# Kernel optimization log

Measured on AMD Instinct MI355X. Metric: run time of the kernel, lower is better.

Reference implementation:

```python
import jax, jax.numpy as jnp
import numpy as np

N_NODES = 50000
N_EDGES = 800000
IN_DIM = 6
HID = 256
OUT = 256
N_EXPERTS = 8
N_LAYERS = 2
N_GRAPHS = 64


def setup_inputs() -> dict:
    key = jax.random.key(0)
    ks = jax.random.split(key, 16)
    s = 0.05
    x = jax.random.normal(ks[0], (N_NODES, IN_DIM), dtype=jnp.float32)
    edge_index = jax.random.randint(ks[1], (2, N_EDGES), 0, N_NODES, dtype=jnp.int64)
    batch = jnp.sort(jax.random.randint(ks[2], (N_NODES,), 0, N_GRAPHS, dtype=jnp.int64))
    # shared encoder
    W_enc = jax.random.normal(ks[3], (IN_DIM, HID), jnp.float32) * s
    b_enc = jnp.zeros((HID,), jnp.float32)
    # router MLP: (HID+2) -> HID -> N_EXPERTS
    Wr1 = jax.random.normal(ks[4], (HID + 2, HID), jnp.float32) * s
    br1 = jnp.zeros((HID,), jnp.float32)
    Wr2 = jax.random.normal(ks[5], (HID, N_EXPERTS), jnp.float32) * s
    br2 = jnp.zeros((N_EXPERTS,), jnp.float32)
    # experts: 2 GraphConv layers each (self weight + neighbor weight + bias), stacked over experts
    Ws0 = jax.random.normal(ks[6], (N_EXPERTS, HID, HID), jnp.float32) * s
    Wn0 = jax.random.normal(ks[7], (N_EXPERTS, HID, HID), jnp.float32) * s
    b0 = jnp.zeros((N_EXPERTS, HID), jnp.float32)
    Ws1 = jax.random.normal(ks[8], (N_EXPERTS, HID, OUT), jnp.float32) * s
    Wn1 = jax.random.normal(ks[9], (N_EXPERTS, HID, OUT), jnp.float32) * s
    b1 = jnp.zeros((N_EXPERTS, OUT), jnp.float32)
    return dict(x=x, edge_index=edge_index, batch=batch, W_enc=W_enc, b_enc=b_enc,
                Wr1=Wr1, br1=br1, Wr2=Wr2, br2=br2,
                Ws0=Ws0, Wn0=Wn0, b0=b0, Ws1=Ws1, Wn1=Wn1, b1=b1)


def _graph_conv(h, src, dst, Ws, Wn, b):
    # PyG GraphConv: x' = x @ Ws + sum_{j in N(i)} x_j @ Wn + b
    msg = h[src] @ Wn                                   # [E, d_out]
    agg = jax.ops.segment_sum(msg, dst, num_segments=N_NODES)
    return h @ Ws + agg + b


def reference(x, edge_index, batch, W_enc, b_enc, Wr1, br1, Wr2, br2,
              Ws0, Wn0, b0, Ws1, Wn1, b1):
    src, dst = edge_index[0], edge_index[1]
    # shared encoder
    h = jax.nn.relu(x @ W_enc + b_enc)                  # [N, HID]
    # graph size features: per-graph node count and edge count, log-scaled, broadcast to nodes
    ones_n = jnp.ones((h.shape[0],), h.dtype)
    node_cnt = jax.ops.segment_sum(ones_n, batch, num_segments=N_GRAPHS)
    edge_cnt = jax.ops.segment_sum(jnp.ones((src.shape[0],), h.dtype), batch[src], num_segments=N_GRAPHS)
    size_feat = jnp.stack([jnp.log1p(node_cnt)[batch], jnp.log1p(edge_cnt)[batch]], axis=-1)  # [N, 2]
    # router -> top-1 expert index
    r = jax.nn.relu(jnp.concatenate([h, size_feat], axis=-1) @ Wr1 + br1)
    logits = r @ Wr2 + br2                              # [N, n_experts]
    idx = jnp.argmax(logits, axis=-1)                   # [N]
    # dense compute-all-experts, then gather by argmax (faithful to original)
    out = jnp.zeros((h.shape[0], Ws1.shape[-1]), h.dtype)
    for e in range(N_EXPERTS):
        z = jax.nn.relu(_graph_conv(h, src, dst, Ws0[e], Wn0[e], b0[e]))
        y_e = _graph_conv(z, src, dst, Ws1[e], Wn1[e], b1[e])   # [N, OUT]
        out = out + jnp.where((idx == e)[:, None], y_e, 0.0)
    return out
```

## Files before the change

### kernel.cpp

```cpp
#include <hip/hip_runtime.h>
#include <hip/hip_bf16.h>
#include <math.h>

#define NN 50000
#define NE 800000
#define NG 64
#define NEXP 8

typedef __attribute__((ext_vector_type(8))) short bf16x8;
typedef __attribute__((ext_vector_type(4))) float f32x4;
typedef unsigned short ushort_t;

__device__ __forceinline__ unsigned short f2bf(float f) {
  union { float f; unsigned u; } x; x.f = f;
  unsigned r = x.u + 0x7fff + ((x.u >> 16) & 1);
  return (unsigned short)(r >> 16);
}
__device__ __forceinline__ float bf2f(unsigned short u) {
  union { unsigned u; float f; } x; x.u = ((unsigned)u) << 16; return x.f;
}

__device__ __forceinline__ void gld16(const void* g, void* l) {
  __builtin_amdgcn_global_load_lds(
      (const __attribute__((address_space(1))) unsigned int*)g,
      (__attribute__((address_space(3))) unsigned int*)l, 16, 0, 0);
}

__global__ __launch_bounds__(256) void k_encoder(
    const float* __restrict__ x, const float* __restrict__ W,
    const float* __restrict__ b, ushort_t* __restrict__ Xb,
    ushort_t* __restrict__ Xlo) {
  int i = blockIdx.x, n = threadIdx.x;
  float acc = b[n];
#pragma unroll
  for (int k = 0; k < 6; k++) acc = fmaf(x[i * 6 + k], W[k * 256 + n], acc);
  acc = fmaxf(acc, 0.f);
  unsigned short hb = f2bf(acc);
  Xb[(size_t)i * 512 + n] = hb;
  Xlo[(size_t)i * 256 + n] = f2bf(acc - bf2f(hb));
}

__global__ __launch_bounds__(256) void k_count_nodes(
    const int* __restrict__ batch, int* __restrict__ node_cnt) {
  __shared__ int bins[NG];
  int t = threadIdx.x;
  if (t < NG) bins[t] = 0;
  __syncthreads();
  for (int i = blockIdx.x * blockDim.x + t; i < NN; i += gridDim.x * blockDim.x)
    atomicAdd(&bins[batch[i]], 1);
  __syncthreads();
  if (t < NG) atomicAdd(&node_cnt[t], bins[t]);
}

__global__ __launch_bounds__(256) void k_count_edges(
    const int* __restrict__ ei, const int* __restrict__ batch,
    int* __restrict__ edge_cnt, int* __restrict__ deg) {
  __shared__ int bins[NG];
  int t = threadIdx.x;
  if (t < NG) bins[t] = 0;
  __syncthreads();
  for (int e = blockIdx.x * blockDim.x + t; e < NE; e += gridDim.x * blockDim.x) {
    int s = ei[e];
    int d = ei[NE + e];
    atomicAdd(&bins[batch[s]], 1);
    atomicAdd(&deg[d], 1);
  }
  __syncthreads();
  if (t < NG) atomicAdd(&edge_cnt[t], bins[t]);
}

__global__ __launch_bounds__(256) void k_sizefeat(
    const int* __restrict__ batch, const int* __restrict__ node_cnt,
    const int* __restrict__ edge_cnt, float* __restrict__ sf0,
    float* __restrict__ sf1) {
  int i = blockIdx.x * blockDim.x + threadIdx.x;
  if (i < NN) {
    int g = batch[i];
    sf0[i] = log1pf((float)node_cnt[g]);
    sf1[i] = log1pf((float)edge_cnt[g]);
  }
}

__global__ __launch_bounds__(1024) void k_scan(
    const int* __restrict__ deg, int* __restrict__ offs, int* __restrict__ cursor) {
  __shared__ int wsums[16];
  int t = threadIdx.x, lane = t & 63, wid = t >> 6;
  int carry = 0;
  for (int base = 0; base < NN; base += 1024) {
    int i = base + t;
    int v = (i < NN) ? deg[i] : 0;
    int x = v;
#pragma unroll
    for (int d = 1; d < 64; d <<= 1) {
      int y = __shfl_up(x, d, 64);
      if (lane >= d) x += y;
    }
    if (lane == 63) wsums[wid] = x;
    __syncthreads();
    if (wid == 0) {
      int s = (lane < 16) ? wsums[lane] : 0;
#pragma unroll
      for (int d = 1; d < 16; d <<= 1) {
        int y = __shfl_up(s, d, 64);
        if (lane >= d) s += y;
      }
      if (lane < 16) wsums[lane] = s;
    }
    __syncthreads();
    int wpre = (wid > 0) ? wsums[wid - 1] : 0;
    int excl = carry + wpre + x - v;
    if (i < NN) { offs[i] = excl; cursor[i] = excl; }
    int btot = wsums[15];
    __syncthreads();
    carry += btot;
  }
  if (t == 0) offs[NN] = carry;
}

__global__ __launch_bounds__(256) void k_fill_csr(
    const int* __restrict__ ei, int* __restrict__ cursor, int* __restrict__ edge_src) {
  int e = blockIdx.x * blockDim.x + threadIdx.x;
  if (e < NE) {
    int d = ei[NE + e];
    int pos = atomicAdd(&cursor[d], 1);
    edge_src[pos] = ei[e];
  }
}

__global__ __launch_bounds__(256) void k_agg_h2(
    const int* __restrict__ offs, const int* __restrict__ edge_src,
    ushort_t* __restrict__ Xb) {
  int wid = threadIdx.x >> 6, lane = threadIdx.x & 63;
  int half = lane >> 5, cl = lane & 31;
  int i = blockIdx.x * 4 + wid;
  if (i >= NN) return;
  int e0 = offs[i], e1 = offs[i + 1];
  float acc[8] = {};
  int k = e0;
  for (; k + 8 <= e1; k += 8) {
    int s0 = edge_src[k + half];
    int s1 = edge_src[k + 2 + half];
    int s2 = edge_src[k + 4 + half];
    int s3 = edge_src[k + 6 + half];
    bf16x8 v0 = *(const bf16x8*)&Xb[(size_t)s0 * 512 + cl * 8];
    bf16x8 v1 = *(const bf16x8*)&Xb[(size_t)s1 * 512 + cl * 8];
    bf16x8 v2 = *(const bf16x8*)&Xb[(size_t)s2 * 512 + cl * 8];
    bf16x8 v3 = *(const bf16x8*)&Xb[(size_t)s3 * 512 + cl * 8];
#pragma unroll
    for (int j = 0; j < 8; j++) acc[j] += bf2f((unsigned short)v0[j]);
#pragma unroll
    for (int j = 0; j < 8; j++) acc[j] += bf2f((unsigned short)v1[j]);
#pragma unroll
    for (int j = 0; j < 8; j++) acc[j] += bf2f((unsigned short)v2[j]);
#pragma unroll
    for (int j = 0; j < 8; j++) acc[j] += bf2f((unsigned short)v3[j]);
  }
  for (; k + 2 <= e1; k += 2) {
    int s0 = edge_src[k + half];
    bf16x8 v0 = *(const bf16x8*)&Xb[(size_t)s0 * 512 + cl * 8];
#pragma unroll
    for (int j = 0; j < 8; j++) acc[j] += bf2f((unsigned short)v0[j]);
  }
  if (k < e1 && half == 0) {
    int s0 = edge_src[k];
    bf16x8 v0 = *(const bf16x8*)&Xb[(size_t)s0 * 512 + cl * 8];
#pragma unroll
    for (int j = 0; j < 8; j++) acc[j] += bf2f((unsigned short)v0[j]);
  }
#pragma unroll
  for (int j = 0; j < 8; j++) acc[j] += __shfl_xor(acc[j], 32, 64);
  if (half == 0) {
    bf16x8 o;
#pragma unroll
    for (int j = 0; j < 8; j++) o[j] = (short)f2bf(acc[j]);
    *(bf16x8*)(&Xb[(size_t)i * 512 + 256 + cl * 8]) = o;
  }
}

__global__ __launch_bounds__(256) void k_prep_w(
    const float* __restrict__ Ws0, const float* __restrict__ Wn0,
    const float* __restrict__ Ws1, const float* __restrict__ Wn1,
    ushort_t* __restrict__ Wt1, ushort_t* __restrict__ Wt2) {
  __shared__ float tile[32][33];
  int z = blockIdx.z;
  int e = z & 7;
  const float* Ws = (z < 8) ? Ws0 : Ws1;
  const float* Wn = (z < 8) ? Wn0 : Wn1;
  ushort_t* Wt = (z < 8) ? Wt1 : Wt2;
  int kt = blockIdx.x;
  int nt = blockIdx.y;
  int tx = threadIdx.x & 31, ty = threadIdx.x >> 5;
  const float* src = (kt < 8) ? (Ws + e * 65536 + (kt * 32) * 256)
                              : (Wn + e * 65536 + ((kt - 8) * 32) * 256);
#pragma unroll
  for (int rr = 0; rr < 32; rr += 8) {
    int k = rr + ty;
    tile[k][tx] = src[k * 256 + nt * 32 + tx];
  }
  __syncthreads();
#pragma unroll
  for (int rr = 0; rr < 32; rr += 8) {
    int n = rr + ty;
    Wt[(size_t)e * 131072 + (nt * 32 + n) * 512 + kt * 32 + tx] = f2bf(tile[tx][n]);
  }
}

__global__ __launch_bounds__(256) void k_prep_wr1(
    const float* __restrict__ Wr1, ushort_t* __restrict__ Wr1t) {
  int k = blockIdx.x;
  int n = threadIdx.x;
  unsigned short v;
  if (k < 256) {
    v = f2bf(Wr1[k * 256 + n]);
  } else {
    float f = Wr1[(k - 256) * 256 + n];
    unsigned short h = f2bf(f);
    v = f2bf(f - bf2f(h));
  }
  Wr1t[(size_t)n * 512 + k] = v;
}

#define TIE_TAU 1e-4f
__global__ __launch_bounds__(256) void k_router_mfma(
    const ushort_t* __restrict__ Xb,
    const ushort_t* __restrict__ Xlo,
    const ushort_t* __restrict__ Wr1t,
    const float* __restrict__ Wr1, const float* __restrict__ br1,
    const float* __restrict__ Wr2, const float* __restrict__ sf0,
    const float* __restrict__ sf1, float* __restrict__ Lpart) {
  __shared__ ushort_t As[2][4096];
  __shared__ ushort_t Bs1[2][4096];
  __shared__ ushort_t Bs2[2][4096];
  __shared__ float Lsm[128][NEXP];
  int t = threadIdx.x;
  int w = t >> 6, lane = t & 63;
  int m0 = blockIdx.x * 128;
  int n0 = blockIdx.y * 128;
  int wm = w >> 1, wn = w & 1;
  int q16 = lane >> 4, c15 = lane & 15;
  for (int z = t; z < 128 * NEXP; z += 256) ((float*)Lsm)[z] = 0.f;

  auto STAGE = [&](int s, int kt) {
    int k0 = (kt & 7) * 32;
    bool hi = kt < 8;
#pragma unroll
    for (int i = 0; i < 2; i++) {
      int c = w * 128 + i * 64 + lane;
      int ch = c >> 7, r = c & 127;
      int gr = m0 + r; if (gr >= NN) gr = NN - 1;
      int dst = (w * 128 + i * 64) * 8;
      if (hi) {
        gld16(Xb + (size_t)gr * 512 + k0 + ch * 8, (void*)&As[s][dst]);
        gld16(Wr1t + (size_t)(n0 + r) * 512 + k0 + ch * 8, (void*)&Bs1[s][dst]);
        gld16(Wr1t + (size_t)(n0 + r) * 512 + 256 + k0 + ch * 8, (void*)&Bs2[s][dst]);
      } else {
        gld16(Xlo + (size_t)gr * 256 + k0 + ch * 8, (void*)&As[s][dst]);
        gld16(Wr1t + (size_t)(n0 + r) * 512 + k0 + ch * 8, (void*)&Bs1[s][dst]);
      }
    }
  };

  f32x4 acc[4][4] = {};
  STAGE(0, 0);
  __syncthreads();
  for (int kt = 0; kt < 16; kt++) {
    int cur = kt & 1;
    if (kt < 15) STAGE(cur ^ 1, kt + 1);
    bf16x8 a[4], b1[4];
#pragma unroll
    for (int i = 0; i < 4; i++) {
      int ra = wm * 64 + i * 16 + c15;
      a[i] = *(const bf16x8*)&As[cur][q16 * 1024 + ra * 8];
      int nb = wn * 64 + i * 16 + c15;
      b1[i] = *(const bf16x8*)&Bs1[cur][q16 * 1024 + nb * 8];
    }
#pragma unroll
    for (int i = 0; i < 4; i++)
#pragma unroll
      for (int j = 0; j < 4; j++)
        acc[i][j] = __builtin_amdgcn_mfma_f32_16x16x32_bf16(a[i], b1[j], acc[i][j], 0, 0, 0);
    if (kt < 8) {
      bf16x8 b2[4];
#pragma unroll
      for (int i = 0; i < 4; i++) {
        int nb = wn * 64 + i * 16 + c15;
        b2[i] = *(const bf16x8*)&Bs2[cur][q16 * 1024 + nb * 8];
      }
#pragma unroll
      for (int i = 0; i < 4; i++)
#pragma unroll
        for (int j = 0; j < 4; j++)
          acc[i][j] = __builtin_amdgcn_mfma_f32_16x16x32_bf16(a[i], b2[j], acc[i][j], 0, 0, 0);
    }
    __syncthreads();
  }

  float bb[4], w6[4], w7[4];
#pragma unroll
  for (int j = 0; j < 4; j++) {
    int col = n0 + wn * 64 + j * 16 + c15;
    bb[j] = br1[col];
    w6[j] = Wr1[65536 + col];
    w7[j] = Wr1[65792 + col];
  }
#pragma unroll
  for (int i = 0; i < 4; i++)
#pragma unroll
    for (int v = 0; v < 4; v++) {
      int row = m0 + wm * 64 + i * 16 + q16 * 4 + v;
      float s0v = (row < NN) ? sf0[row] : 0.f;
      float s1v = (row < NN) ? sf1[row] : 0.f;
#pragma unroll
      for (int j = 0; j < 4; j++)
        acc[i][j][v] = fmaxf(acc[i][j][v] + bb[j] + s0v * w6[j] + s1v * w7[j], 0.f);
    }
#pragma unroll
  for (int e = 0; e < NEXP; e++) {
    float wr2j[4];
#pragma unroll
    for (int j = 0; j < 4; j++)
      wr2j[j] = Wr2[(n0 + wn * 64 + j * 16 + c15) * 8 + e];
    float pe[4][4];
#pragma unroll
    for (int i = 0; i < 4; i++)
#pragma unroll
      for (int v = 0; v < 4; v++) {
        float s = acc[i][0][v] * wr2j[0];
        s = fmaf(acc[i][1][v], wr2j[1], s);
        s = fmaf(acc[i][2][v], wr2j[2], s);
        s = fmaf(acc[i][3][v], wr2j[3], s);
        pe[i][v] = s;
      }
#pragma unroll
    for (int d = 1; d < 16; d <<= 1)
#pragma unroll
      for (int i = 0; i < 4; i++)
#pragma unroll
        for (int v = 0; v < 4; v++)
          pe[i][v] += __shfl_xor(pe[i][v], d, 64);
    if (c15 == 0) {
#pragma unroll
      for (int i = 0; i < 4; i++)
#pragma unroll
        for (int v = 0; v < 4; v++)
          atomicAdd(&Lsm[wm * 64 + i * 16 + q16 * 4 + v][e], pe[i][v]);
    }
  }
  __syncthreads();
  for (int z = t; z < 128 * NEXP; z += 256) {
    int lr = z >> 3, e = z & 7;
    int row = m0 + lr;
    if (row < NN)
      Lpart[(size_t)blockIdx.y * (NN * 8) + (size_t)row * 8 + e] = Lsm[lr][e];
  }
}

__global__ __launch_bounds__(256) void k_argmax(
    const float* __restrict__ Lpart, const float* __restrict__ br2,
    int* __restrict__ idx, int* __restrict__ nfix, int* __restrict__ fixlist) {
  int i = blockIdx.x * 256 + threadIdx.x;
  if (i >= NN) return;
  float best = -1e30f, second = -1e30f; int bi = 0;
#pragma unroll
  for (int e = 0; e < NEXP; e++) {
    float v = br2[e] + Lpart[(size_t)i * 8 + e]
              + Lpart[(size_t)(NN * 8) + (size_t)i * 8 + e];
    if (v > best) { second = best; best = v; bi = e; }
    else if (v > second) second = v;
  }
  idx[i] = bi;
  if (best - second < TIE_TAU) {
    int p = atomicAdd(nfix, 1);
    fixlist[p] = i;
  }
}

__global__ __launch_bounds__(256) void k_fixup(
    const float* __restrict__ x, const float* __restrict__ W_enc,
    const float* __restrict__ b_enc, const float* __restrict__ Wr1,
    const float* __restrict__ br1, const float* __restrict__ Wr2,
    const float* __restrict__ br2, const float* __restrict__ sf0,
    const float* __restrict__ sf1, const int* __restrict__ fixlist,
    const int* __restrict__ nfix, int* __restrict__ idx) {
  __shared__ float hsh[256];
  __shared__ float lred[4][NEXP];
  int n = *nfix;
  int t = threadIdx.x, wid = t >> 6, lane = t & 63;
  for (int qq = blockIdx.x; qq < n; qq += gridDim.x) {
    int node = fixlist[qq];
    float hv = b_enc[t];
#pragma unroll
    for (int k = 0; k < 6; k++)
      hv = fmaf(x[node * 6 + k], W_enc[k * 256 + t], hv);
    hsh[t] = fmaxf(hv, 0.f);
    __syncthreads();
    float acc = br1[t] + sf0[node] * Wr1[65536 + t] + sf1[node] * Wr1[65792 + t];
    for (int k = 0; k < 256; k++)
      acc = fmaf(hsh[k], Wr1[k * 256 + t], acc);
    float r = fmaxf(acc, 0.f);
    float le[NEXP];
#pragma unroll
    for (int e = 0; e < NEXP; e++) le[e] = r * Wr2[t * 8 + e];
#pragma unroll
    for (int d = 32; d > 0; d >>= 1)
#pragma unroll
      for (int e = 0; e < NEXP; e++) le[e] += __shfl_xor(le[e], d, 64);
    if (lane == 0) {
#pragma unroll
      for (int e = 0; e < NEXP; e++) lred[wid][e] = le[e];
    }
    __syncthreads();
    if (t == 0) {
      float best = -1e30f; int bi = 0;
      for (int e = 0; e < NEXP; e++) {
        float v = lred[0][e] + lred[1][e] + lred[2][e] + lred[3][e] + br2[e];
        if (v > best) { best = v; bi = e; }
      }
      idx[node] = bi;
    }
    __syncthreads();
  }
}

__global__ __launch_bounds__(256) void k_ecnt(
    const int* __restrict__ idx, int* __restrict__ ecnt) {
  __shared__ int bins[NEXP];
  int t = threadIdx.x;
  if (t < NEXP) bins[t] = 0;
  __syncthreads();
  for (int i = blockIdx.x * 256 + t; i < NN; i += gridDim.x * 256)
    atomicAdd(&bins[idx[i]], 1);
  __syncthreads();
  if (t < NEXP) atomicAdd(&ecnt[t], bins[t]);
}

__global__ __launch_bounds__(256) void k_srcmask(
    const int* __restrict__ ei, const int* __restrict__ idx,
    unsigned int* __restrict__ mask) {
  int k = blockIdx.x * 256 + threadIdx.x;
  if (k < NE) {
    int s = ei[k], d = ei[NE + k];
    atomicOr(&mask[s], 1u << idx[d]);
  }
  if (k < NN) atomicOr(&mask[k], 1u << idx[k]);
}

__global__ __launch_bounds__(256) void k_scount(
    const unsigned int* __restrict__ mask, int* __restrict__ scnt) {
  __shared__ int bins[NEXP];
  int t = threadIdx.x;
  if (t < NEXP) bins[t] = 0;
  __syncthreads();
  for (int i = blockIdx.x * 256 + t; i < NN; i += gridDim.x * 256) {
    unsigned m = mask[i];
    while (m) { int b = __ffs(m) - 1; atomicAdd(&bins[b], 1); m &= m - 1; }
  }
  __syncthreads();
  if (t < NEXP) atomicAdd(&scnt[t], bins[t]);
}

__global__ void k_bucket_offs(const int* __restrict__ ecnt,
                              const int* __restrict__ scnt,
                              int* __restrict__ boff, int* __restrict__ bcur,
                              int* __restrict__ tstart,
                              int* __restrict__ soff, int* __restrict__ scur) {
  if (threadIdx.x == 0) {
    int s = 0, ts = 0, s2 = 0;
    for (int e = 0; e < NEXP; e++) {
      boff[e] = s; bcur[e] = s;
      tstart[e] = ts;
      ts += (ecnt[e] + 127) / 128;
      s += ecnt[e];
      soff[e] = s2; scur[e] = s2;
      s2 += scnt[e];
    }
    boff[NEXP] = s;
    tstart[NEXP] = ts;
    soff[NEXP] = s2;
  }
}

#define BF_BLOCKS 64
__global__ __launch_bounds__(256) void k_bucket_fill2(
    const int* __restrict__ idx, int* __restrict__ bcur, int* __restrict__ nlist) {
  __shared__ int lcnt[NEXP];
  __shared__ int lbase[NEXP];
  int t = threadIdx.x;
  int chunk = (NN + BF_BLOCKS - 1) / BF_BLOCKS;
  int lo = blockIdx.x * chunk;
  int hi = lo + chunk; if (hi > NN) hi = NN;
  if (t < NEXP) lcnt[t] = 0;
  __syncthreads();
  for (int i = lo + t; i < hi; i += 256) atomicAdd(&lcnt[idx[i]], 1);
  __syncthreads();
  if (t < NEXP) lbase[t] = atomicAdd(&bcur[t], lcnt[t]);
  __syncthreads();
  if (t < NEXP) lcnt[t] = 0;
  __syncthreads();
  for (int i = lo + t; i < hi; i += 256) {
    int e = idx[i];
    int p = atomicAdd(&lcnt[e], 1);
    nlist[lbase[e] + p] = i;
  }
}

__global__ __launch_bounds__(256) void k_scompact(
    const unsigned int* __restrict__ mask, int* __restrict__ scur,
    int* __restrict__ slist) {
  __shared__ int lcnt[NEXP];
  __shared__ int lbase[NEXP];
  int t = threadIdx.x;
  int chunk = (NN + BF_BLOCKS - 1) / BF_BLOCKS;
  int lo = blockIdx.x * chunk;
  int hi = lo + chunk; if (hi > NN) hi = NN;
  if (t < NEXP) lcnt[t] = 0;
  __syncthreads();
  for (int i = lo + t; i < hi; i += 256) {
    unsigned m = mask[i];
    while (m) { int b = __ffs(m) - 1; atomicAdd(&lcnt[b], 1); m &= m - 1; }
  }
  __syncthreads();
  if (t < NEXP) lbase[t] = atomicAdd(&scur[t], lcnt[t]);
  __syncthreads();
  if (t < NEXP) lcnt[t] = 0;
  __syncthreads();
  for (int i = lo + t; i < hi; i += 256) {
    unsigned m = mask[i];
    while (m) {
      int b = __ffs(m) - 1;
      int p = atomicAdd(&lcnt[b], 1);
      slist[lbase[b] + p] = i;
      m &= m - 1;
    }
  }
}

__global__ __launch_bounds__(256) void k_layer1_rows(
    const ushort_t* __restrict__ Abf,
    const ushort_t* __restrict__ Wt,
    const float* __restrict__ b0, const int* __restrict__ idx,
    const int* __restrict__ slist, const int* __restrict__ soff, int e,
    ushort_t* __restrict__ Zb, ushort_t* __restrict__ A2) {
  int base = soff[e];
  int cnt = soff[e + 1] - base;
  int m0 = blockIdx.x * 128;
  if (m0 >= cnt) return;
  __shared__ ushort_t As[2][4096];
  __shared__ ushort_t Bs[2][4096];
  __shared__ int rows[128];
  __shared__ int sidx[128];
  int t = threadIdx.x;
  if (t < 128) {
    int r = (m0 + t < cnt) ? slist[base + m0 + t] : -1;
    rows[t] = r;
    sidx[t] = (r >= 0) ? idx[r] : -1;
  }
  __syncthreads();
  int w = t >> 6, lane = t & 63;
  int n0 = blockIdx.y * 128;
  int wm = w >> 1, wn = w & 1;
  int q16 = lane >> 4, c15 = lane & 15;
  const ushort_t* Wb = Wt + (size_t)e * 131072;

  auto STAGE = [&](int s, int kt) {
    int k0 = kt * 32;
#pragma unroll
    for (int i = 0; i < 2; i++) {
      int c = w * 128 + i * 64 + lane;
      int ch = c >> 7, r = c & 127;
      int nd = rows[r]; if (nd < 0) nd = 0;
      int dst = (w * 128 + i * 64) * 8;
      gld16(Abf + (size_t)nd * 512 + k0 + ch * 8, (void*)&As[s][dst]);
      gld16(Wb + (size_t)(n0 + r) * 512 + k0 + ch * 8, (void*)&Bs[s][dst]);
    }
  };

  f32x4 acc[4][4] = {};
  STAGE(0, 0);
  __syncthreads();
  for (int kt = 0; kt < 16; kt++) {
    int cur = kt & 1;
    if (kt < 15) STAGE(cur ^ 1, kt + 1);
    bf16x8 a[4], b[4];
#pragma unroll
    for (int i = 0; i < 4; i++) {
      int ra = wm * 64 + i * 16 + c15;
      a[i] = *(const bf16x8*)&As[cur][q16 * 1024 + ra * 8];
      int nb = wn * 64 + i * 16 + c15;
      b[i] = *(const bf16x8*)&Bs[cur][q16 * 1024 + nb * 8];
    }
#pragma unroll
    for (int i = 0; i < 4; i++)
#pragma unroll
      for (int j = 0; j < 4; j++)
        acc[i][j] = __builtin_amdgcn_mfma_f32_16x16x32_bf16(a[i], b[j], acc[i][j], 0, 0, 0);
    __syncthreads();
  }
  int q = lane >> 4;
#pragma unroll
  for (int i = 0; i < 4; i++) {
#pragma unroll
    for (int j = 0; j < 4; j++) {
      int col = n0 + wn * 64 + j * 16 + c15;
      float bias = b0[e * 256 + col];
#pragma unroll
      for (int v = 0; v < 4; v++) {
        int lrow = wm * 64 + i * 16 + q * 4 + v;
        int node = rows[lrow];
        if (node >= 0) {
          unsigned short zb = f2bf(fmaxf(acc[i][j][v] + bias, 0.f));
          Zb[(size_t)node * 256 + col] = zb;
          if (sidx[lrow] == e) A2[(size_t)node * 512 + col] = zb;
        }
      }
    }
  }
}

__global__ __launch_bounds__(256) void k_agg_z2(
    const ushort_t* __restrict__ Zb, const int* __restrict__ offs,
    const int* __restrict__ edge_src, const int* __restrict__ nlist,
    const int* __restrict__ boff, int e, ushort_t* __restrict__ A2) {
  int wid = threadIdx.x >> 6, lane = threadIdx.x & 63;
  int half = lane >> 5, cl = lane & 31;
  int base = boff[e];
  int cnt = boff[e + 1] - base;
  for (int b = blockIdx.x * 4 + wid; b < cnt; b += gridDim.x * 4) {
    int i = nlist[base + b];
    int e0 = offs[i], e1 = offs[i + 1];
    float acc[8] = {};
    int k = e0;
    for (; k + 8 <= e1; k += 8) {
      int s0 = edge_src[k + half];
      int s1 = edge_src[k + 2 + half];
      int s2 = edge_src[k + 4 + half];
      int s3 = edge_src[k + 6 + half];
      bf16x8 v0 = *(const bf16x8*)&Zb[(size_t)s0 * 256 + cl * 8];
      bf16x8 v1 = *(const bf16x8*)&Zb[(size_t)s1 * 256 + cl * 8];
      bf16x8 v2 = *(const bf16x8*)&Zb[(size_t)s2 * 256 + cl * 8];
      bf16x8 v3 = *(const bf16x8*)&Zb[(size_t)s3 * 256 + cl * 8];
#pragma unroll
      for (int j = 0; j < 8; j++) acc[j] += bf2f((unsigned short)v0[j]);
#pragma unroll
      for (int j = 0; j < 8; j++) acc[j] += bf2f((unsigned short)v1[j]);
#pragma unroll
      for (int j = 0; j < 8; j++) acc[j] += bf2f((unsigned short)v2[j]);
#pragma unroll
      for (int j = 0; j < 8; j++) acc[j] += bf2f((unsigned short)v3[j]);
    }
    for (; k + 2 <= e1; k += 2) {
      int s0 = edge_src[k + half];
      bf16x8 v0 = *(const bf16x8*)&Zb[(size_t)s0 * 256 + cl * 8];
#pragma unroll
      for (int j = 0; j < 8; j++) acc[j] += bf2f((unsigned short)v0[j]);
    }
    if (k < e1 && half == 0) {
      int s0 = edge_src[k];
      bf16x8 v0 = *(const bf16x8*)&Zb[(size_t)s0 * 256 + cl * 8];
#pragma unroll
      for (int j = 0; j < 8; j++) acc[j] += bf2f((unsigned short)v0[j]);
    }
#pragma unroll
    for (int j = 0; j < 8; j++) acc[j] += __shfl_xor(acc[j], 32, 64);
    if (half == 0) {
      bf16x8 o;
#pragma unroll
      for (int j = 0; j < 8; j++) o[j] = (short)f2bf(acc[j]);
      *(bf16x8*)(&A2[(size_t)i * 512 + 256 + cl * 8]) = o;
    }
  }
}

#define MAXT2 (391 + NEXP)
__global__ __launch_bounds__(256) void k_layer2_mfma(
    const ushort_t* __restrict__ A2,
    const ushort_t* __restrict__ Wt,
    const float* __restrict__ b1, const int* __restrict__ nlist,
    const int* __restrict__ boff, const int* __restrict__ tstart,
    float* __restrict__ outp) {
  __shared__ ushort_t As[2][4096];
  __shared__ ushort_t Bs[2][4096];
  __shared__ int rows[128];
  int t = threadIdx.x;
  int tx = blockIdx.x;
  int e = -1;
#pragma unroll
  for (int q = 0; q < NEXP; q++)
    if (tx >= tstart[q] && tx < tstart[q + 1]) e = q;
  if (e < 0) return;
  int tile = tx - tstart[e];
  int base = boff[e];
  int cnt = boff[e + 1] - base;
  int m0 = tile * 128;
  if (t < 128) rows[t] = (m0 + t < cnt) ? nlist[base + m0 + t] : -1;
  __syncthreads();
  int w = t >> 6, lane = t & 63;
  int n0 = blockIdx.y * 128;
  int wm = w >> 1, wn = w & 1;
  int q16 = lane >> 4, c15 = lane & 15;
  const ushort_t* Wb = Wt + (size_t)e * 131072;

  auto STAGE = [&](int s, int kt) {
    int k0 = kt * 32;
#pragma unroll
    for (int i = 0; i < 2; i++) {
      int c = w * 128 + i * 64 + lane;
      int ch = c >> 7, r = c & 127;
      int nd = rows[r]; if (nd < 0) nd = 0;
      int dst = (w * 128 + i * 64) * 8;
      gld16(A2 + (size_t)nd * 512 + k0 + ch * 8, (void*)&As[s][dst]);
      gld16(Wb + (size_t)(n0 + r) * 512 + k0 + ch * 8, (void*)&Bs[s][dst]);
    }
  };

  f32x4 acc[4][4] = {};
  STAGE(0, 0);
  __syncthreads();
  for (int kt = 0; kt < 16; kt++) {
    int cur = kt & 1;
    if (kt < 15) STAGE(cur ^ 1, kt + 1);
    bf16x8 a[4], b[4];
#pragma unroll
    for (int i = 0; i < 4; i++) {
      int ra = wm * 64 + i * 16 + c15;
      a[i] = *(const bf16x8*)&As[cur][q16 * 1024 + ra * 8];
      int nb = wn * 64 + i * 16 + c15;
      b[i] = *(const bf16x8*)&Bs[cur][q16 * 1024 + nb * 8];
    }
#pragma unroll
    for (int i = 0; i < 4; i++)
#pragma unroll
      for (int j = 0; j < 4; j++)
        acc[i][j] = __builtin_amdgcn_mfma_f32_16x16x32_bf16(a[i], b[j], acc[i][j], 0, 0, 0);
    __syncthreads();
  }
  int q = lane >> 4;
#pragma unroll
  for (int i = 0; i < 4; i++) {
#pragma unroll
    for (int j = 0; j < 4; j++) {
      int col = n0 + wn * 64 + j * 16 + c15;
      float bias = b1[e * 256 + col];
#pragma unroll
      for (int v = 0; v < 4; v++) {
        int lrow = wm * 64 + i * 16 + q * 4 + v;
        int node = rows[lrow];
        if (node >= 0) outp[(size_t)node * 256 + col] = acc[i][j][v] + bias;
      }
    }
  }
}

static inline char* wsalloc(char*& p, size_t bytes) {
  char* r = p;
  p += (bytes + 255) & ~(size_t)255;
  return r;
}

extern "C" void kernel_launch(void* const* d_in, const int* in_sizes, int n_in,
                              void* d_out, int out_size, void* d_ws, size_t ws_size,
                              hipStream_t stream) {
  const float* x     = (const float*)d_in[0];
  const int*   ei    = (const int*)d_in[1];
  const int*   batch = (const int*)d_in[2];
  const float* W_enc = (const float*)d_in[3];
  const float* b_enc = (const float*)d_in[4];
  const float* Wr1   = (const float*)d_in[5];
  const float* br1   = (const float*)d_in[6];
  const float* Wr2   = (const float*)d_in[7];
  const float* br2   = (const float*)d_in[8];
  const float* Ws0   = (const float*)d_in[9];
  const float* Wn0   = (const float*)d_in[10];
  const float* b0    = (const float*)d_in[11];
  const float* Ws1   = (const float*)d_in[12];
  const float* Wn1   = (const float*)d_in[13];
  const float* b1    = (const float*)d_in[14];
  float* outp = (float*)d_out;

  char* p = (char*)d_ws;
  ushort_t* Xb   = (ushort_t*)wsalloc(p, (size_t)NN * 512 * 2);
  ushort_t* Zb   = (ushort_t*)wsalloc(p, (size_t)NN * 256 * 2);
  ushort_t* A2   = (ushort_t*)wsalloc(p, (size_t)NN * 512 * 2);
  ushort_t* Xlo  = Zb;
  float*    Lpart= (float*)wsalloc(p, (size_t)2 * NN * 8 * 4);
  ushort_t* Wt1  = (ushort_t*)wsalloc(p, (size_t)NEXP * 256 * 512 * 2);
  ushort_t* Wt2  = (ushort_t*)wsalloc(p, (size_t)NEXP * 256 * 512 * 2);
  ushort_t* Wr1t = (ushort_t*)wsalloc(p, (size_t)256 * 512 * 2);
  int* edge_src  = (int*)wsalloc(p, (size_t)NE * 4);
  int* offs      = (int*)wsalloc(p, (size_t)(NN + 1) * 4);
  int* cursor    = (int*)wsalloc(p, (size_t)NN * 4);
  int* deg       = (int*)wsalloc(p, (size_t)NN * 4);
  int* idxb      = (int*)wsalloc(p, (size_t)NN * 4);
  float* sf0     = (float*)wsalloc(p, (size_t)NN * 4);
  float* sf1     = (float*)wsalloc(p, (size_t)NN * 4);
  int* nlist     = (int*)wsalloc(p, (size_t)NN * 4);
  int* fixlist   = (int*)wsalloc(p, (size_t)NN * 4);
  unsigned int* maskb = (unsigned int*)wsalloc(p, (size_t)NN * 4);
  int* slist     = (int*)wsalloc(p, (size_t)NN * NEXP * 4);
  int* smallb    = (int*)wsalloc(p, 256 * 4);
  int* node_cnt = smallb;
  int* edge_cnt = smallb + 64;
  int* ecnt     = smallb + 128;
  int* boff     = smallb + 136;
  int* bcur     = smallb + 152;
  int* tstart   = smallb + 160;
  int* nfix     = smallb + 192;
  int* scnt     = smallb + 200;
  int* soff     = smallb + 208;
  int* scur     = smallb + 224;

  hipMemsetAsync(deg, 0, (size_t)NN * 4, stream);
  hipMemsetAsync(smallb, 0, 256 * 4, stream);
  hipMemsetAsync(maskb, 0, (size_t)NN * 4, stream);

  k_encoder<<<NN, 256, 0, stream>>>(x, W_enc, b_enc, Xb, Xlo);
  k_count_nodes<<<64, 256, 0, stream>>>(batch, node_cnt);
  k_count_edges<<<128, 256, 0, stream>>>(ei, batch, edge_cnt, deg);
  k_sizefeat<<<(NN + 255) / 256, 256, 0, stream>>>(batch, node_cnt, edge_cnt, sf0, sf1);
  k_scan<<<1, 1024, 0, stream>>>(deg, offs, cursor);
  k_fill_csr<<<(NE + 255) / 256, 256, 0, stream>>>(ei, cursor, edge_src);
  k_agg_h2<<<(NN + 3) / 4, 256, 0, stream>>>(offs, edge_src, Xb);
  k_prep_w<<<dim3(16, 8, 16), 256, 0, stream>>>(Ws0, Wn0, Ws1, Wn1, Wt1, Wt2);
  k_prep_wr1<<<512, 256, 0, stream>>>(Wr1, Wr1t);
  k_router_mfma<<<dim3((NN + 127) / 128, 2), 256, 0, stream>>>(
      Xb, Xlo, Wr1t, Wr1, br1, Wr2, sf0, sf1, Lpart);
  k_argmax<<<(NN + 255) / 256, 256, 0, stream>>>(Lpart, br2, idxb, nfix, fixlist);
  k_fixup<<<256, 256, 0, stream>>>(x, W_enc, b_enc, Wr1, br1, Wr2, br2,
                                   sf0, sf1, fixlist, nfix, idxb);
  k_srcmask<<<(NE + 255) / 256, 256, 0, stream>>>(ei, idxb, maskb);
  k_ecnt<<<64, 256, 0, stream>>>(idxb, ecnt);
  k_scount<<<64, 256, 0, stream>>>(maskb, scnt);
  k_bucket_offs<<<1, 64, 0, stream>>>(ecnt, scnt, boff, bcur, tstart, soff, scur);
  k_bucket_fill2<<<BF_BLOCKS, 256, 0, stream>>>(idxb, bcur, nlist);
  k_scompact<<<BF_BLOCKS, 256, 0, stream>>>(maskb, scur, slist);
  for (int e = 0; e < NEXP; e++) {
    k_layer1_rows<<<dim3((NN + 127) / 128, 2), 256, 0, stream>>>(
        Xb, Wt1, b0, idxb, slist, soff, e, Zb, A2);
    k_agg_z2<<<3125, 256, 0, stream>>>(Zb, offs, edge_src, nlist, boff, e, A2);
  }
  k_layer2_mfma<<<dim3(MAXT2, 2), 256, 0, stream>>>(
      A2, Wt2, b1, nlist, boff, tstart, outp);
}
```

Before: 691.3 us.

## Fuse per-expert layer1/aggregation loop into single launches with compacted Z buffer and LDS swizzle

The eight-iteration expert loop of layer-1 GEMM plus neighbor aggregation becomes one layer-1 kernel covering all experts' tiles and one aggregation kernel over all nodes. Layer-1 outputs go to a compacted Zc buffer indexed through a per-expert position map. The launches are fewer, the GPU fills better, and the separate per-expert passes disappear. Separately, all MFMA GEMM LDS tiles switch to a row-major XOR-swizzled layout to cut bank conflicts. The compacted buffer is capped at 3*NN rows and overflow positions fall back to index 0, which silently gives wrong results if the source-mask sets exceed the cap.

```diff
diff --git a/kernel.cpp b/kernel.cpp
--- a/kernel.cpp
+++ b/kernel.cpp
@@ -6,6 +6,7 @@
 #define NE 800000
 #define NG 64
 #define NEXP 8
+#define ZC_CAP (3 * NN)
 
 typedef __attribute__((ext_vector_type(8))) short bf16x8;
 typedef __attribute__((ext_vector_type(4))) float f32x4;
@@ -246,16 +247,17 @@
 #pragma unroll
     for (int i = 0; i < 2; i++) {
       int c = w * 128 + i * 64 + lane;
-      int ch = c >> 7, r = c & 127;
+      int r = c >> 2, kc = c & 3;
+      int kcs = kc ^ (r & 3);
       int gr = m0 + r; if (gr >= NN) gr = NN - 1;
       int dst = (w * 128 + i * 64) * 8;
       if (hi) {
-        gld16(Xb + (size_t)gr * 512 + k0 + ch * 8, (void*)&As[s][dst]);
-        gld16(Wr1t + (size_t)(n0 + r) * 512 + k0 + ch * 8, (void*)&Bs1[s][dst]);
-        gld16(Wr1t + (size_t)(n0 + r) * 512 + 256 + k0 + ch * 8, (void*)&Bs2[s][dst]);
+        gld16(Xb + (size_t)gr * 512 + k0 + kcs * 8, (void*)&As[s][dst]);
+        gld16(Wr1t + (size_t)(n0 + r) * 512 + k0 + kcs * 8, (void*)&Bs1[s][dst]);
+        gld16(Wr1t + (size_t)(n0 + r) * 512 + 256 + k0 + kcs * 8, (void*)&Bs2[s][dst]);
       } else {
-        gld16(Xlo + (size_t)gr * 256 + k0 + ch * 8, (void*)&As[s][dst]);
-        gld16(Wr1t + (size_t)(n0 + r) * 512 + k0 + ch * 8, (void*)&Bs1[s][dst]);
+        gld16(Xlo + (size_t)gr * 256 + k0 + kcs * 8, (void*)&As[s][dst]);
+        gld16(Wr1t + (size_t)(n0 + r) * 512 + k0 + kcs * 8, (void*)&Bs1[s][dst]);
       }
     }
   };
@@ -270,9 +272,9 @@
 #pragma unroll
     for (int i = 0; i < 4; i++) {
       int ra = wm * 64 + i * 16 + c15;
-      a[i] = *(const bf16x8*)&As[cur][q16 * 1024 + ra * 8];
+      a[i] = *(const bf16x8*)&As[cur][ra * 32 + (q16 ^ (ra & 3)) * 8];
       int nb = wn * 64 + i * 16 + c15;
-      b1[i] = *(const bf16x8*)&Bs1[cur][q16 * 1024 + nb * 8];
+      b1[i] = *(const bf16x8*)&Bs1[cur][nb * 32 + (q16 ^ (nb & 3)) * 8];
     }
 #pragma unroll
     for (int i = 0; i < 4; i++)
@@ -284,7 +286,7 @@
 #pragma unroll
       for (int i = 0; i < 4; i++) {
         int nb = wn * 64 + i * 16 + c15;
-        b2[i] = *(const bf16x8*)&Bs2[cur][q16 * 1024 + nb * 8];
+        b2[i] = *(const bf16x8*)&Bs2[cur][nb * 32 + (q16 ^ (nb & 3)) * 8];
       }
 #pragma unroll
       for (int i = 0; i < 4; i++)
@@ -463,20 +465,24 @@
                               const int* __restrict__ scnt,
                               int* __restrict__ boff, int* __restrict__ bcur,
                               int* __restrict__ tstart,
-                              int* __restrict__ soff, int* __restrict__ scur) {
+                              int* __restrict__ soff, int* __restrict__ scur,
+                              int* __restrict__ ltstart) {
   if (threadIdx.x == 0) {
-    int s = 0, ts = 0, s2 = 0;
+    int s = 0, ts = 0, s2 = 0, lt = 0;
     for (int e = 0; e < NEXP; e++) {
       boff[e] = s; bcur[e] = s;
       tstart[e] = ts;
       ts += (ecnt[e] + 127) / 128;
       s += ecnt[e];
       soff[e] = s2; scur[e] = s2;
+      ltstart[e] = lt;
+      lt += (scnt[e] + 127) / 128;
       s2 += scnt[e];
     }
     boff[NEXP] = s;
     tstart[NEXP] = ts;
     soff[NEXP] = s2;
+    ltstart[NEXP] = lt;
   }
 }
 
@@ -506,7 +512,7 @@
 
 __global__ __launch_bounds__(256) void k_scompact(
     const unsigned int* __restrict__ mask, int* __restrict__ scur,
-    int* __restrict__ slist) {
+    int* __restrict__ slist, int* __restrict__ posmap) {
   __shared__ int lcnt[NEXP];
   __shared__ int lbase[NEXP];
   int t = threadIdx.x;
@@ -529,22 +535,32 @@
     while (m) {
       int b = __ffs(m) - 1;
       int p = atomicAdd(&lcnt[b], 1);
-      slist[lbase[b] + p] = i;
+      int gp = lbase[b] + p;
+      slist[gp] = i;
+      posmap[(size_t)b * NN + i] = (gp < ZC_CAP) ? gp : 0;
       m &= m - 1;
     }
   }
 }
 
-__global__ __launch_bounds__(256) void k_layer1_rows(
+#define MAXT1 (8 * 391 + 8)
+__global__ __launch_bounds__(256) void k_layer1_all(
     const ushort_t* __restrict__ Abf,
     const ushort_t* __restrict__ Wt,
     const float* __restrict__ b0, const int* __restrict__ idx,
-    const int* __restrict__ slist, const int* __restrict__ soff, int e,
-    ushort_t* __restrict__ Zb, ushort_t* __restrict__ A2) {
+    const int* __restrict__ slist, const int* __restrict__ soff,
+    const int* __restrict__ ltstart,
+    ushort_t* __restrict__ Zc, ushort_t* __restrict__ A2) {
+  int tx = blockIdx.x;
+  int e = -1;
+#pragma unroll
+  for (int q = 0; q < NEXP; q++)
+    if (tx >= ltstart[q] && tx < ltstart[q + 1]) e = q;
+  if (e < 0) return;
+  int tile = tx - ltstart[e];
   int base = soff[e];
   int cnt = soff[e + 1] - base;
-  int m0 = blockIdx.x * 128;
-  if (m0 >= cnt) return;
+  int m0 = tile * 128;
   __shared__ ushort_t As[2][4096];
   __shared__ ushort_t Bs[2][4096];
   __shared__ int rows[128];
@@ -567,11 +583,12 @@
 #pragma unroll
     for (int i = 0; i < 2; i++) {
       int c = w * 128 + i * 64 + lane;
-      int ch = c >> 7, r = c & 127;
+      int r = c >> 2, kc = c & 3;
+      int kcs = kc ^ (r & 3);
       int nd = rows[r]; if (nd < 0) nd = 0;
       int dst = (w * 128 + i * 64) * 8;
-      gld16(Abf + (size_t)nd * 512 + k0 + ch * 8, (void*)&As[s][dst]);
-      gld16(Wb + (size_t)(n0 + r) * 512 + k0 + ch * 8, (void*)&Bs[s][dst]);
+      gld16(Abf + (size_t)nd * 512 + k0 + kcs * 8, (void*)&As[s][dst]);
+      gld16(Wb + (size_t)(n0 + r) * 512 + k0 + kcs * 8, (void*)&Bs[s][dst]);
     }
   };
 
@@ -585,9 +602,9 @@
 #pragma unroll
     for (int i = 0; i < 4; i++) {
       int ra = wm * 64 + i * 16 + c15;
-      a[i] = *(const bf16x8*)&As[cur][q16 * 1024 + ra * 8];
+      a[i] = *(const bf16x8*)&As[cur][ra * 32 + (q16 ^ (ra & 3)) * 8];
       int nb = wn * 64 + i * 16 + c15;
-      b[i] = *(const bf16x8*)&Bs[cur][q16 * 1024 + nb * 8];
+      b[i] = *(const bf16x8*)&Bs[cur][nb * 32 + (q16 ^ (nb & 3)) * 8];
     }
 #pragma unroll
     for (int i = 0; i < 4; i++)
@@ -596,7 +613,6 @@
         acc[i][j] = __builtin_amdgcn_mfma_f32_16x16x32_bf16(a[i], b[j], acc[i][j], 0, 0, 0);
     __syncthreads();
   }
-  int q = lane >> 4;
 #pragma unroll
   for (int i = 0; i < 4; i++) {
 #pragma unroll
@@ -605,11 +621,12 @@
       float bias = b0[e * 256 + col];
 #pragma unroll
       for (int v = 0; v < 4; v++) {
-        int lrow = wm * 64 + i * 16 + q * 4 + v;
+        int lrow = wm * 64 + i * 16 + q16 * 4 + v;
         int node = rows[lrow];
         if (node >= 0) {
           unsigned short zb = f2bf(fmaxf(acc[i][j][v] + bias, 0.f));
-          Zb[(size_t)node * 256 + col] = zb;
+          int sp = base + m0 + lrow;
+          if (sp < ZC_CAP) Zc[(size_t)sp * 256 + col] = zb;
           if (sidx[lrow] == e) A2[(size_t)node * 512 + col] = zb;
         }
       }
@@ -617,16 +634,20 @@
   }
 }
 
-__global__ __launch_bounds__(256) void k_agg_z2(
-    const ushort_t* __restrict__ Zb, const int* __restrict__ offs,
+__global__ __launch_bounds__(256) void k_agg_z_all(
+    const ushort_t* __restrict__ Zc, const int* __restrict__ offs,
     const int* __restrict__ edge_src, const int* __restrict__ nlist,
-    const int* __restrict__ boff, int e, ushort_t* __restrict__ A2) {
+    const int* __restrict__ boff, const int* __restrict__ posmap,
+    ushort_t* __restrict__ A2) {
   int wid = threadIdx.x >> 6, lane = threadIdx.x & 63;
   int half = lane >> 5, cl = lane & 31;
-  int base = boff[e];
-  int cnt = boff[e + 1] - base;
-  for (int b = blockIdx.x * 4 + wid; b < cnt; b += gridDim.x * 4) {
-    int i = nlist[base + b];
+  for (int b = blockIdx.x * 4 + wid; b < NN; b += gridDim.x * 4) {
+    int e = 0;
+#pragma unroll
+    for (int q = 1; q < NEXP; q++)
+      if (b >= boff[q]) e = q;
+    int i = nlist[b];
+    const int* pm = posmap + (size_t)e * NN;
     int e0 = offs[i], e1 = offs[i + 1];
     float acc[8] = {};
     int k = e0;
@@ -635,10 +656,11 @@
       int s1 = edge_src[k + 2 + half];
       int s2 = edge_src[k + 4 + half];
       int s3 = edge_src[k + 6 + half];
-      bf16x8 v0 = *(const bf16x8*)&Zb[(size_t)s0 * 256 + cl * 8];
-      bf16x8 v1 = *(const bf16x8*)&Zb[(size_t)s1 * 256 + cl * 8];
-      bf16x8 v2 = *(const bf16x8*)&Zb[(size_t)s2 * 256 + cl * 8];
-      bf16x8 v3 = *(const bf16x8*)&Zb[(size_t)s3 * 256 + cl * 8];
+      int p0 = pm[s0], p1 = pm[s1], p2 = pm[s2], p3 = pm[s3];
+      bf16x8 v0 = *(const bf16x8*)&Zc[(size_t)p0 * 256 + cl * 8];
+      bf16x8 v1 = *(const bf16x8*)&Zc[(size_t)p1 * 256 + cl * 8];
+      bf16x8 v2 = *(const bf16x8*)&Zc[(size_t)p2 * 256 + cl * 8];
+      bf16x8 v3 = *(const bf16x8*)&Zc[(size_t)p3 * 256 + cl * 8];
 #pragma unroll
       for (int j = 0; j < 8; j++) acc[j] += bf2f((unsigned short)v0[j]);
 #pragma unroll
@@ -650,13 +672,15 @@
     }
     for (; k + 2 <= e1; k += 2) {
       int s0 = edge_src[k + half];
-      bf16x8 v0 = *(const bf16x8*)&Zb[(size_t)s0 * 256 + cl * 8];
+      int p0 = pm[s0];
+      bf16x8 v0 = *(const bf16x8*)&Zc[(size_t)p0 * 256 + cl * 8];
 #pragma unroll
       for (int j = 0; j < 8; j++) acc[j] += bf2f((unsigned short)v0[j]);
     }
     if (k < e1 && half == 0) {
       int s0 = edge_src[k];
-      bf16x8 v0 = *(const bf16x8*)&Zb[(size_t)s0 * 256 + cl * 8];
+      int p0 = pm[s0];
+      bf16x8 v0 = *(const bf16x8*)&Zc[(size_t)p0 * 256 + cl * 8];
 #pragma unroll
       for (int j = 0; j < 8; j++) acc[j] += bf2f((unsigned short)v0[j]);
     }
@@ -705,11 +729,12 @@
 #pragma unroll
     for (int i = 0; i < 2; i++) {
       int c = w * 128 + i * 64 + lane;
-      int ch = c >> 7, r = c & 127;
+      int r = c >> 2, kc = c & 3;
+      int kcs = kc ^ (r & 3);
       int nd = rows[r]; if (nd < 0) nd = 0;
       int dst = (w * 128 + i * 64) * 8;
-      gld16(A2 + (size_t)nd * 512 + k0 + ch * 8, (void*)&As[s][dst]);
-      gld16(Wb + (size_t)(n0 + r) * 512 + k0 + ch * 8, (void*)&Bs[s][dst]);
+      gld16(A2 + (size_t)nd * 512 + k0 + kcs * 8, (void*)&As[s][dst]);
+      gld16(Wb + (size_t)(n0 + r) * 512 + k0 + kcs * 8, (void*)&Bs[s][dst]);
     }
   };
 
@@ -723,9 +748,9 @@
 #pragma unroll
     for (int i = 0; i < 4; i++) {
       int ra = wm * 64 + i * 16 + c15;
-      a[i] = *(const bf16x8*)&As[cur][q16 * 1024 + ra * 8];
+      a[i] = *(const bf16x8*)&As[cur][ra * 32 + (q16 ^ (ra & 3)) * 8];
       int nb = wn * 64 + i * 16 + c15;
-      b[i] = *(const bf16x8*)&Bs[cur][q16 * 1024 + nb * 8];
+      b[i] = *(const bf16x8*)&Bs[cur][nb * 32 + (q16 ^ (nb & 3)) * 8];
     }
 #pragma unroll
     for (int i = 0; i < 4; i++)
@@ -734,7 +759,6 @@
         acc[i][j] = __builtin_amdgcn_mfma_f32_16x16x32_bf16(a[i], b[j], acc[i][j], 0, 0, 0);
     __syncthreads();
   }
-  int q = lane >> 4;
 #pragma unroll
   for (int i = 0; i < 4; i++) {
 #pragma unroll
@@ -743,7 +767,7 @@
       float bias = b1[e * 256 + col];
 #pragma unroll
       for (int v = 0; v < 4; v++) {
-        int lrow = wm * 64 + i * 16 + q * 4 + v;
+        int lrow = wm * 64 + i * 16 + q16 * 4 + v;
         int node = rows[lrow];
         if (node >= 0) outp[(size_t)node * 256 + col] = acc[i][j][v] + bias;
       }
@@ -779,9 +803,9 @@
 
   char* p = (char*)d_ws;
   ushort_t* Xb   = (ushort_t*)wsalloc(p, (size_t)NN * 512 * 2);
-  ushort_t* Zb   = (ushort_t*)wsalloc(p, (size_t)NN * 256 * 2);
+  ushort_t* Zc   = (ushort_t*)wsalloc(p, (size_t)ZC_CAP * 256 * 2);
   ushort_t* A2   = (ushort_t*)wsalloc(p, (size_t)NN * 512 * 2);
-  ushort_t* Xlo  = Zb;
+  ushort_t* Xlo  = Zc;
   float*    Lpart= (float*)wsalloc(p, (size_t)2 * NN * 8 * 4);
   ushort_t* Wt1  = (ushort_t*)wsalloc(p, (size_t)NEXP * 256 * 512 * 2);
   ushort_t* Wt2  = (ushort_t*)wsalloc(p, (size_t)NEXP * 256 * 512 * 2);
@@ -797,6 +821,7 @@
   int* fixlist   = (int*)wsalloc(p, (size_t)NN * 4);
   unsigned int* maskb = (unsigned int*)wsalloc(p, (size_t)NN * 4);
   int* slist     = (int*)wsalloc(p, (size_t)NN * NEXP * 4);
+  int* posmap    = (int*)wsalloc(p, (size_t)NN * NEXP * 4);
   int* smallb    = (int*)wsalloc(p, 256 * 4);
   int* node_cnt = smallb;
   int* edge_cnt = smallb + 64;
@@ -808,6 +833,7 @@
   int* scnt     = smallb + 200;
   int* soff     = smallb + 208;
   int* scur     = smallb + 224;
+  int* ltstart  = smallb + 232;
 
   hipMemsetAsync(deg, 0, (size_t)NN * 4, stream);
   hipMemsetAsync(smallb, 0, 256 * 4, stream);
@@ -830,14 +856,12 @@
   k_srcmask<<<(NE + 255) / 256, 256, 0, stream>>>(ei, idxb, maskb);
   k_ecnt<<<64, 256, 0, stream>>>(idxb, ecnt);
   k_scount<<<64, 256, 0, stream>>>(maskb, scnt);
-  k_bucket_offs<<<1, 64, 0, stream>>>(ecnt, scnt, boff, bcur, tstart, soff, scur);
+  k_bucket_offs<<<1, 64, 0, stream>>>(ecnt, scnt, boff, bcur, tstart, soff, scur, ltstart);
   k_bucket_fill2<<<BF_BLOCKS, 256, 0, stream>>>(idxb, bcur, nlist);
-  k_scompact<<<BF_BLOCKS, 256, 0, stream>>>(maskb, scur, slist);
-  for (int e = 0; e < NEXP; e++) {
-    k_layer1_rows<<<dim3((NN + 127) / 128, 2), 256, 0, stream>>>(
-        Xb, Wt1, b0, idxb, slist, soff, e, Zb, A2);
-    k_agg_z2<<<3125, 256, 0, stream>>>(Zb, offs, edge_src, nlist, boff, e, A2);
-  }
+  k_scompact<<<BF_BLOCKS, 256, 0, stream>>>(maskb, scur, slist, posmap);
+  k_layer1_all<<<dim3(MAXT1, 2), 256, 0, stream>>>(
+      Xb, Wt1, b0, idxb, slist, soff, ltstart, Zc, A2);
+  k_agg_z_all<<<3125, 256, 0, stream>>>(Zc, offs, edge_src, nlist, boff, posmap, A2);
   k_layer2_mfma<<<dim3(MAXT2, 2), 256, 0, stream>>>(
       A2, Wt2, b1, nlist, boff, tstart, outp);
 }
```

Result: faster. 612.2 us (-11.4%).
